# Performance work log

Measured on AMD Instinct MI355X. Metric: run time of the kernel, lower is better.

## Reference

```python
import jax, jax.numpy as jnp
import numpy as np

N_HEAD = 16
D_HEAD = 64
D_MODEL = 1024
LN_EPS = 1e-5


def layer_norm(x, gamma, beta):
    mu = jnp.mean(x, axis=-1, keepdims=True)
    var = jnp.mean((x - mu) ** 2, axis=-1, keepdims=True)
    return (x - mu) * jax.lax.rsqrt(var + LN_EPS) * gamma + beta


def setup_inputs() -> dict:
    key = jax.random.key(0)
    ks = jax.random.split(key, 6)
    B, T = 2, 2048
    inp = jax.random.normal(ks[0], (B, T, D_MODEL), dtype=jnp.float32)
    # qkv_net: Linear(d_model, 3*n_head*d_head)
    W_qkv = jax.random.normal(ks[1], (3 * N_HEAD * D_HEAD, D_MODEL), dtype=jnp.float32) * (D_MODEL ** -0.5)
    b_qkv = jax.random.normal(ks[2], (3 * N_HEAD * D_HEAD,), dtype=jnp.float32) * 0.02
    # o_net: Linear(n_head*d_head, d_model, bias=False)
    W_o = jax.random.normal(ks[3], (D_MODEL, N_HEAD * D_HEAD), dtype=jnp.float32) * ((N_HEAD * D_HEAD) ** -0.5)
    gamma = jnp.ones((D_MODEL,), dtype=jnp.float32)
    beta = jnp.zeros((D_MODEL,), dtype=jnp.float32)
    return {"inp": inp, "W_qkv": W_qkv, "b_qkv": b_qkv, "W_o": W_o, "gamma": gamma, "beta": beta}


def reference(inp, W_qkv, b_qkv, W_o, gamma, beta):
    B, T, D = inp.shape
    H, dh = N_HEAD, D_HEAD
    scale = 1.0 / (dh ** 0.5)

    qkv = inp @ W_qkv.T + b_qkv                      # (B, T, 3*H*dh)
    head_q, head_k, head_v = jnp.split(qkv, 3, axis=2)
    # (B, T, H, dh) -> (B, H, T, dh)
    q = head_q.reshape(B, T, H, dh).transpose(0, 2, 1, 3)
    k = head_k.reshape(B, T, H, dh).transpose(0, 2, 1, 3)
    v = head_v.reshape(B, T, H, dh).transpose(0, 2, 1, 3)

    attn_score = jnp.einsum('bhqd,bhkd->bhqk', q, k) * scale  # (B, H, T, T)
    attn_prob = jax.nn.softmax(attn_score, axis=-1)           # dropatt is identity in eval
    attn_vec = jnp.einsum('bhqk,bhkd->bhqd', attn_prob, v)    # (B, H, T, dh)

    # Faithful to original: (B*H, T, dh) batch-major buffer is VIEWED as (H, B, T, dh)
    attn_vec = attn_vec.reshape(H, B, T, dh)
    attn_vec = attn_vec.transpose(1, 2, 0, 3).reshape(B, T, H * dh)

    attn_out = attn_vec @ W_o.T                                # dropout identity in eval
    return layer_norm(inp + attn_out, gamma, beta)
```

## Files before the change

### kernel.cpp

```cpp
#include <hip/hip_runtime.h>
#include <hip/hip_bf16.h>
#include <stdint.h>

typedef __bf16 bf16_t;
typedef __bf16 bf16x8 __attribute__((ext_vector_type(8)));
typedef __bf16 bf16x4 __attribute__((ext_vector_type(4)));
typedef float floatx4 __attribute__((ext_vector_type(4)));

#define QSCALE 0.180336879f

__device__ static inline void gll16(const void* g, void* l) {
    __builtin_amdgcn_global_load_lds((const __attribute__((address_space(1))) void*)g,
                                     (__attribute__((address_space(3))) void*)l, 16, 0, 0);
}

__global__ __launch_bounds__(256) void cvt_all(const float* __restrict__ inp,
                                               const float* __restrict__ wqkv,
                                               const float* __restrict__ wo,
                                               bf16_t* __restrict__ o_inp,
                                               bf16_t* __restrict__ o_wqkv,
                                               bf16_t* __restrict__ o_wo) {
    int blk = blockIdx.x;
    const float* src;
    bf16_t* dst;
    if (blk < 4096)      { src = inp;  dst = o_inp; }
    else if (blk < 7168) { src = wqkv; dst = o_wqkv; blk -= 4096; }
    else                 { src = wo;   dst = o_wo;   blk -= 7168; }
    int i = blk * 256 + threadIdx.x;
    float4 v = ((const float4*)src)[i];
    bf16x4 o;
    o[0] = (bf16_t)v.x; o[1] = (bf16_t)v.y; o[2] = (bf16_t)v.z; o[3] = (bf16_t)v.w;
    ((bf16x4*)dst)[i] = o;
}

__global__ __launch_bounds__(256, 3)
void gemm_qkv(const bf16_t* __restrict__ A, const bf16_t* __restrict__ Bw,
              const float* __restrict__ bias,
              bf16_t* __restrict__ qk, bf16_t* __restrict__ vT) {
    constexpr int K = 1024;
    __shared__ bf16_t lA[128 * 32];
    __shared__ bf16_t lB[128 * 32];
    const int tid  = threadIdx.x;
    const int lane = tid & 63, wave = tid >> 6;
    const int quad = lane >> 4, l16 = lane & 15;
    const int wy = wave >> 1, wx = wave & 1;
    const int bm = blockIdx.y * 128, bn = blockIdx.x * 128;

    const int c0 = tid, c1 = tid + 256;
    const bf16_t* Ap0 = A + (size_t)(bm + (c0 >> 2)) * K + (c0 & 3) * 8;
    const bf16_t* Ap1 = A + (size_t)(bm + (c1 >> 2)) * K + (c1 & 3) * 8;
    const bf16_t* Bp0 = Bw + (size_t)(bn + (c0 >> 2)) * K + (c0 & 3) * 8;
    const bf16_t* Bp1 = Bw + (size_t)(bn + (c1 >> 2)) * K + (c1 & 3) * 8;
    bf16_t* dA0 = &lA[(wave * 64) * 8];
    bf16_t* dA1 = &lA[(256 + wave * 64) * 8];
    bf16_t* dB0 = &lB[(wave * 64) * 8];
    bf16_t* dB1 = &lB[(256 + wave * 64) * 8];

    floatx4 acc[4][4] = {};

    for (int kt = 0; kt < K; kt += 32) {
        __syncthreads();
        gll16(Ap0 + kt, dA0);
        gll16(Ap1 + kt, dA1);
        gll16(Bp0 + kt, dB0);
        gll16(Bp1 + kt, dB1);
        __syncthreads();
        bf16x8 af[4], bfr[4];
#pragma unroll
        for (int i = 0; i < 4; i++) {
            af[i]  = *(const bf16x8*)(lA + (wy * 64 + i * 16 + l16) * 32 + quad * 8);
            bfr[i] = *(const bf16x8*)(lB + (wx * 64 + i * 16 + l16) * 32 + quad * 8);
        }
#pragma unroll
        for (int i = 0; i < 4; i++)
#pragma unroll
            for (int j = 0; j < 4; j++)
                acc[i][j] = __builtin_amdgcn_mfma_f32_16x16x32_bf16(af[i], bfr[j], acc[i][j], 0, 0, 0);
    }

    const bool is_v = (bn >= 2048);
#pragma unroll
    for (int j = 0; j < 4; j++) {
        const int n = bn + wx * 64 + j * 16 + l16;
        const float bv = bias[n];
        const bool isq = (n < 1024);
#pragma unroll
        for (int i = 0; i < 4; i++) {
            const int mbase = bm + wy * 64 + i * 16 + quad * 4;
            if (!is_v) {
#pragma unroll
                for (int r = 0; r < 4; r++) {
                    float c = acc[i][j][r] + bv;
                    if (isq) c *= QSCALE;
                    qk[(size_t)(mbase + r) * 2048 + n] = (bf16_t)c;
                }
            } else {
                const int nn = n - 2048;
                const int b  = mbase >> 11;
                const int t  = mbase & 2047;
                const int vrow = b * 1024 + nn;
                const int pcol = (t & ~31) | (((t >> 2) & 3) << 3) | (((t >> 4) & 1) << 2);
                bf16x4 pack;
#pragma unroll
                for (int r = 0; r < 4; r++) pack[r] = (bf16_t)(acc[i][j][r] + bv);
                *(bf16x4*)(vT + (size_t)vrow * 2048 + pcol) = pack;
            }
        }
    }
}

__global__ __launch_bounds__(256, 4)
void attn_kernel(const bf16_t* __restrict__ qk, const bf16_t* __restrict__ vT,
                 bf16_t* __restrict__ Opart, float* __restrict__ lpart) {
    __shared__ bf16_t Kbuf[2][64 * 64];
    __shared__ bf16_t Vbuf[2][64 * 64];
    const int tid  = threadIdx.x;
    const int lane = tid & 63, wave = tid >> 6;
    const int quad = lane >> 4, l16 = lane & 15;
    const int bid = blockIdx.x;
    const int s    = bid & 63;
    const int hl   = ((s & 7) << 2) | ((s >> 3) & 3);
    const int half = (s >> 5) & 1;
    const int qt   = bid >> 6;
    const int b = hl >> 4, h = hl & 15;
    const int kt0 = half * 1024;

    const bf16_t* Qbase = qk + (size_t)(b * 2048 + qt * 128 + wave * 32) * 2048 + h * 64;
    const bf16_t* Kbase = qk + (size_t)(b * 2048) * 2048 + 1024 + h * 64;
    const bf16_t* Vbase = vT + (size_t)(hl * 64) * 2048;

    const int srow = tid >> 2, sc8 = (tid & 3) * 8;
    const bf16_t* KgA = Kbase + (size_t)(kt0 + srow) * 2048 + sc8;
    const bf16_t* KgB = KgA + 32;
    const bf16_t* VgA = Vbase + (size_t)srow * 2048 + kt0 + sc8;
    const bf16_t* VgB = VgA + 32;
    const int wbase = wave * 512;

    bf16x8 qf[2][2];
#pragma unroll
    for (int rt = 0; rt < 2; rt++)
#pragma unroll
        for (int kc = 0; kc < 2; kc++)
            qf[rt][kc] = *(const bf16x8*)(Qbase + (size_t)(rt * 16 + l16) * 2048 + kc * 32 + quad * 8);

    floatx4 accO[2][4] = {};
    float lacc[2] = {0.f, 0.f};

    gll16(KgA, &Kbuf[0][wbase]);
    gll16(KgB, &Kbuf[0][2048 + wbase]);
    gll16(VgA, &Vbuf[0][wbase]);
    gll16(VgB, &Vbuf[0][2048 + wbase]);

    for (int it = 0; it < 16; ++it) {
        const int cur = it & 1, nxt = cur ^ 1;
        __syncthreads();
        if (it < 15) {
            const size_t ko = (size_t)(it + 1) * 64 * 2048;
            const int    vo = (it + 1) * 64;
            gll16(KgA + ko, &Kbuf[nxt][wbase]);
            gll16(KgB + ko, &Kbuf[nxt][2048 + wbase]);
            gll16(VgA + vo, &Vbuf[nxt][wbase]);
            gll16(VgB + vo, &Vbuf[nxt][2048 + wbase]);
        }
        floatx4 st[2][4] = {};
#pragma unroll
        for (int nt = 0; nt < 4; nt++) {
            bf16x8 k0 = *(const bf16x8*)&Kbuf[cur][(nt * 16 + l16) * 32 + quad * 8];
            bf16x8 k1 = *(const bf16x8*)&Kbuf[cur][2048 + (nt * 16 + l16) * 32 + quad * 8];
            st[0][nt] = __builtin_amdgcn_mfma_f32_16x16x32_bf16(k0, qf[0][0], st[0][nt], 0, 0, 0);
            st[0][nt] = __builtin_amdgcn_mfma_f32_16x16x32_bf16(k1, qf[0][1], st[0][nt], 0, 0, 0);
            st[1][nt] = __builtin_amdgcn_mfma_f32_16x16x32_bf16(k0, qf[1][0], st[1][nt], 0, 0, 0);
            st[1][nt] = __builtin_amdgcn_mfma_f32_16x16x32_bf16(k1, qf[1][1], st[1][nt], 0, 0, 0);
        }
#pragma unroll
        for (int kc2 = 0; kc2 < 2; kc2++) {
            bf16x8 vf[4];
#pragma unroll
            for (int ct = 0; ct < 4; ct++)
                vf[ct] = *(const bf16x8*)&Vbuf[cur][kc2 * 2048 + (ct * 16 + l16) * 32 + quad * 8];
#pragma unroll
            for (int rt = 0; rt < 2; rt++) {
                bf16x8 pf;
                float ls = 0.f;
#pragma unroll
                for (int j = 0; j < 8; j++) {
                    float p = __builtin_amdgcn_exp2f(st[rt][kc2 * 2 + (j >> 2)][j & 3]);
                    ls += p;
                    pf[j] = (bf16_t)p;
                }
                lacc[rt] += ls;
#pragma unroll
                for (int ct = 0; ct < 4; ct++)
                    accO[rt][ct] = __builtin_amdgcn_mfma_f32_16x16x32_bf16(pf, vf[ct], accO[rt][ct], 0, 0, 0);
            }
        }
    }

    float lsum[2];
#pragma unroll
    for (int rt = 0; rt < 2; rt++) {
        float l = lacc[rt];
        l += __shfl_xor(l, 16);
        l += __shfl_xor(l, 32);
        lsum[rt] = l;
    }
    const int b2 = hl & 1;
    const int colb = hl >> 1;
    const int rowb = b2 * 2048 + qt * 128 + wave * 32;
    bf16_t* outb = Opart + (size_t)half * (4096 * 1024) + (size_t)rowb * 1024 + colb * 64;
#pragma unroll
    for (int rt = 0; rt < 2; rt++)
#pragma unroll
        for (int ct = 0; ct < 4; ct++)
#pragma unroll
            for (int r = 0; r < 4; r++)
                outb[(size_t)(rt * 16 + quad * 4 + r) * 1024 + ct * 16 + l16] = (bf16_t)(accO[rt][ct][r]);
    if (quad == 0) {
#pragma unroll
        for (int rt = 0; rt < 2; rt++)
            lpart[half * 65536 + (rowb + rt * 16 + l16) * 16 + colb] = lsum[rt];
    }
}

__global__ __launch_bounds__(256, 4)
void gemm_o(const bf16_t* __restrict__ Op, const float* __restrict__ lp,
            const bf16_t* __restrict__ Bw, float* __restrict__ out) {
    constexpr int K = 1024;
    __shared__ bf16_t lA[64 * 32];
    __shared__ bf16_t lB[128 * 32];
    const int tid  = threadIdx.x;
    const int lane = tid & 63, wave = tid >> 6;
    const int quad = lane >> 4, l16 = lane & 15;
    const int wy = wave >> 1, wx = wave & 1;
    const int bm = blockIdx.y * 64, bn = blockIdx.x * 128;

    const int ca = tid;
    const int arow = bm + (ca >> 2);
    const int ak   = (ca & 3) * 8;
    const bf16_t* Ap0 = Op + (size_t)arow * 1024 + ak;
    const bf16_t* Ap1 = Ap0 + (size_t)4096 * 1024;
    const float*  lrow = lp + arow * 16;
    const int cb0 = tid, cb1 = tid + 256;
    const bf16_t* Bp0 = Bw + (size_t)(bn + (cb0 >> 2)) * K + (cb0 & 3) * 8;
    const bf16_t* Bp1 = Bw + (size_t)(bn + (cb1 >> 2)) * K + (cb1 & 3) * 8;
    bf16_t* dB0 = &lB[(wave * 64) * 8];
    bf16_t* dB1 = &lB[(256 + wave * 64) * 8];

    floatx4 acc[2][4] = {};
    for (int kt = 0; kt < K; kt += 32) {
        bf16x8 a0 = *(const bf16x8*)(Ap0 + kt);
        bf16x8 a1 = *(const bf16x8*)(Ap1 + kt);
        const int cb = (kt + ak) >> 6;
        const float inv = 1.0f / (lrow[cb] + lrow[65536 + cb]);
        bf16x8 av;
#pragma unroll
        for (int j = 0; j < 8; j++)
            av[j] = (bf16_t)(((float)a0[j] + (float)a1[j]) * inv);
        __syncthreads();
        gll16(Bp0 + kt, dB0);
        gll16(Bp1 + kt, dB1);
        *(bf16x8*)&lA[ca * 8] = av;
        __syncthreads();
        bf16x8 af[2], bfr[4];
#pragma unroll
        for (int i = 0; i < 2; i++)
            af[i] = *(const bf16x8*)(lA + (wy * 32 + i * 16 + l16) * 32 + quad * 8);
#pragma unroll
        for (int j = 0; j < 4; j++)
            bfr[j] = *(const bf16x8*)(lB + (wx * 64 + j * 16 + l16) * 32 + quad * 8);
#pragma unroll
        for (int i = 0; i < 2; i++)
#pragma unroll
            for (int j = 0; j < 4; j++)
                acc[i][j] = __builtin_amdgcn_mfma_f32_16x16x32_bf16(af[i], bfr[j], acc[i][j], 0, 0, 0);
    }
#pragma unroll
    for (int j = 0; j < 4; j++) {
        const int n = bn + wx * 64 + j * 16 + l16;
#pragma unroll
        for (int i = 0; i < 2; i++) {
            const int mbase = bm + wy * 32 + i * 16 + quad * 4;
#pragma unroll
            for (int r = 0; r < 4; r++)
                out[(size_t)(mbase + r) * 1024 + n] = acc[i][j][r];
        }
    }
}

__global__ __launch_bounds__(256)
void ln_kernel(const float* __restrict__ inp, const float* __restrict__ ao,
               const float* __restrict__ gamma, const float* __restrict__ beta,
               float* __restrict__ out) {
    const int row = blockIdx.x, tid = threadIdx.x;
    const int wave = tid >> 6, lane = tid & 63;
    float4 a = ((const float4*)(inp + (size_t)row * 1024))[tid];
    float4 c = ((const float4*)(ao + (size_t)row * 1024))[tid];
    float x0 = a.x + c.x, x1 = a.y + c.y, x2 = a.z + c.z, x3 = a.w + c.w;
    float s = x0 + x1 + x2 + x3;
    float sq = x0 * x0 + x1 * x1 + x2 * x2 + x3 * x3;
#pragma unroll
    for (int mm = 32; mm >= 1; mm >>= 1) {
        s += __shfl_xor(s, mm);
        sq += __shfl_xor(sq, mm);
    }
    __shared__ float rs[4], rq[4];
    if (lane == 0) { rs[wave] = s; rq[wave] = sq; }
    __syncthreads();
    s = rs[0] + rs[1] + rs[2] + rs[3];
    sq = rq[0] + rq[1] + rq[2] + rq[3];
    const float mu = s * (1.0f / 1024.0f);
    const float var = sq * (1.0f / 1024.0f) - mu * mu;
    const float rstd = rsqrtf(var + 1e-5f);
    float4 g = ((const float4*)gamma)[tid], bt = ((const float4*)beta)[tid];
    float4 o;
    o.x = (x0 - mu) * rstd * g.x + bt.x;
    o.y = (x1 - mu) * rstd * g.y + bt.y;
    o.z = (x2 - mu) * rstd * g.z + bt.z;
    o.w = (x3 - mu) * rstd * g.w + bt.w;
    ((float4*)(out + (size_t)row * 1024))[tid] = o;
}

extern "C" void kernel_launch(void* const* d_in, const int* in_sizes, int n_in,
                              void* d_out, int out_size, void* d_ws, size_t ws_size,
                              hipStream_t stream) {
    const float* inp   = (const float*)d_in[0];
    const float* Wqkv  = (const float*)d_in[1];
    const float* bqkv  = (const float*)d_in[2];
    const float* Wo    = (const float*)d_in[3];
    const float* gamma = (const float*)d_in[4];
    const float* beta  = (const float*)d_in[5];
    float* out = (float*)d_out;

    char* ws = (char*)d_ws;
    bf16_t* inp_bf  = (bf16_t*)(ws);
    bf16_t* wqkv_bf = (bf16_t*)(ws + (8u << 20));
    bf16_t* wo_bf   = (bf16_t*)(ws + (14u << 20));
    bf16_t* qk_buf  = (bf16_t*)(ws + (16u << 20));
    bf16_t* vT_buf  = (bf16_t*)(ws + (32u << 20));
    float*  ao_buf  = (float*)(ws + (32u << 20));
    bf16_t* opart   = (bf16_t*)(ws + (48u << 20));
    float*  lpart   = (float*)(ws);

    cvt_all<<<8192, 256, 0, stream>>>(inp, Wqkv, Wo, inp_bf, wqkv_bf, wo_bf);
    gemm_qkv<<<dim3(24, 32), 256, 0, stream>>>(inp_bf, wqkv_bf, bqkv, qk_buf, vT_buf);
    attn_kernel<<<1024, 256, 0, stream>>>(qk_buf, vT_buf, opart, lpart);
    gemm_o<<<dim3(8, 64), 256, 0, stream>>>(opart, lpart, wo_bf, ao_buf);
    ln_kernel<<<4096, 256, 0, stream>>>(inp, ao_buf, gamma, beta, out);
}
```

Baseline: 204.2 us.

## Use packed bf16 conversion, prefetch gemm_o A tiles, store attention output in bf16

Adds a pack8 helper that uses the packed f32-to-bf16 convert builtin when it is available, and applies it in cvt_all, in the attention softmax-to-MFMA path and in gemm_o. gemm_o now loads the next A-operand chunk from global memory after the barrier, so the load overlaps the MFMA work. The o-projection result is also written as bf16 instead of fp32, which halves that intermediate's write and the layer-norm read of it. The bf16 intermediate loses precision before the residual add and layer norm.

```diff
diff --git a/kernel.cpp b/kernel.cpp
--- a/kernel.cpp
+++ b/kernel.cpp
@@ -5,13 +5,33 @@
 typedef __bf16 bf16_t;
 typedef __bf16 bf16x8 __attribute__((ext_vector_type(8)));
 typedef __bf16 bf16x4 __attribute__((ext_vector_type(4)));
+typedef __bf16 bf16x2 __attribute__((ext_vector_type(2)));
 typedef float floatx4 __attribute__((ext_vector_type(4)));
 
 #define QSCALE 0.180336879f
+
+#if __has_builtin(__builtin_amdgcn_cvt_pk_bf16_f32)
+#define HAS_PK_BF16 1
+#endif
 
 __device__ static inline void gll16(const void* g, void* l) {
     __builtin_amdgcn_global_load_lds((const __attribute__((address_space(1))) void*)g,
                                      (__attribute__((address_space(3))) void*)l, 16, 0, 0);
+}
+
+__device__ static inline bf16x8 pack8(const float* p) {
+    bf16x8 o;
+#ifdef HAS_PK_BF16
+#pragma unroll
+    for (int j = 0; j < 4; j++) {
+        bf16x2 t2 = __builtin_amdgcn_cvt_pk_bf16_f32(p[2 * j], p[2 * j + 1]);
+        o[2 * j] = t2[0]; o[2 * j + 1] = t2[1];
+    }
+#else
+#pragma unroll
+    for (int j = 0; j < 8; j++) o[j] = (bf16_t)p[j];
+#endif
+    return o;
 }
 
 __global__ __launch_bounds__(256) void cvt_all(const float* __restrict__ inp,
@@ -28,8 +48,15 @@
     else                 { src = wo;   dst = o_wo;   blk -= 7168; }
     int i = blk * 256 + threadIdx.x;
     float4 v = ((const float4*)src)[i];
+    float p[4] = {v.x, v.y, v.z, v.w};
     bf16x4 o;
-    o[0] = (bf16_t)v.x; o[1] = (bf16_t)v.y; o[2] = (bf16_t)v.z; o[3] = (bf16_t)v.w;
+#ifdef HAS_PK_BF16
+    bf16x2 t0 = __builtin_amdgcn_cvt_pk_bf16_f32(p[0], p[1]);
+    bf16x2 t1 = __builtin_amdgcn_cvt_pk_bf16_f32(p[2], p[3]);
+    o[0] = t0[0]; o[1] = t0[1]; o[2] = t1[0]; o[3] = t1[1];
+#else
+    o[0] = (bf16_t)p[0]; o[1] = (bf16_t)p[1]; o[2] = (bf16_t)p[2]; o[3] = (bf16_t)p[3];
+#endif
     ((bf16x4*)dst)[i] = o;
 }
 
@@ -180,15 +207,15 @@
                 vf[ct] = *(const bf16x8*)&Vbuf[cur][kc2 * 2048 + (ct * 16 + l16) * 32 + quad * 8];
 #pragma unroll
             for (int rt = 0; rt < 2; rt++) {
-                bf16x8 pf;
+                float p[8];
                 float ls = 0.f;
 #pragma unroll
                 for (int j = 0; j < 8; j++) {
-                    float p = __builtin_amdgcn_exp2f(st[rt][kc2 * 2 + (j >> 2)][j & 3]);
-                    ls += p;
-                    pf[j] = (bf16_t)p;
+                    p[j] = __builtin_amdgcn_exp2f(st[rt][kc2 * 2 + (j >> 2)][j & 3]);
+                    ls += p[j];
                 }
                 lacc[rt] += ls;
+                bf16x8 pf = pack8(p);
 #pragma unroll
                 for (int ct = 0; ct < 4; ct++)
                     accO[rt][ct] = __builtin_amdgcn_mfma_f32_16x16x32_bf16(pf, vf[ct], accO[rt][ct], 0, 0, 0);
@@ -224,7 +251,7 @@
 
 __global__ __launch_bounds__(256, 4)
 void gemm_o(const bf16_t* __restrict__ Op, const float* __restrict__ lp,
-            const bf16_t* __restrict__ Bw, float* __restrict__ out) {
+            const bf16_t* __restrict__ Bw, bf16_t* __restrict__ out) {
     constexpr int K = 1024;
     __shared__ bf16_t lA[64 * 32];
     __shared__ bf16_t lB[128 * 32];
@@ -246,21 +273,26 @@
     bf16_t* dB0 = &lB[(wave * 64) * 8];
     bf16_t* dB1 = &lB[(256 + wave * 64) * 8];
 
+    bf16x8 a0 = *(const bf16x8*)(Ap0);
+    bf16x8 a1 = *(const bf16x8*)(Ap1);
+
     floatx4 acc[2][4] = {};
     for (int kt = 0; kt < K; kt += 32) {
-        bf16x8 a0 = *(const bf16x8*)(Ap0 + kt);
-        bf16x8 a1 = *(const bf16x8*)(Ap1 + kt);
         const int cb = (kt + ak) >> 6;
         const float inv = 1.0f / (lrow[cb] + lrow[65536 + cb]);
-        bf16x8 av;
-#pragma unroll
-        for (int j = 0; j < 8; j++)
-            av[j] = (bf16_t)(((float)a0[j] + (float)a1[j]) * inv);
+        float p[8];
+#pragma unroll
+        for (int j = 0; j < 8; j++) p[j] = ((float)a0[j] + (float)a1[j]) * inv;
+        bf16x8 av = pack8(p);
         __syncthreads();
         gll16(Bp0 + kt, dB0);
         gll16(Bp1 + kt, dB1);
         *(bf16x8*)&lA[ca * 8] = av;
         __syncthreads();
+        if (kt + 32 < K) {
+            a0 = *(const bf16x8*)(Ap0 + kt + 32);
+            a1 = *(const bf16x8*)(Ap1 + kt + 32);
+        }
         bf16x8 af[2], bfr[4];
 #pragma unroll
         for (int i = 0; i < 2; i++)
@@ -282,20 +314,21 @@
             const int mbase = bm + wy * 32 + i * 16 + quad * 4;
 #pragma unroll
             for (int r = 0; r < 4; r++)
-                out[(size_t)(mbase + r) * 1024 + n] = acc[i][j][r];
+                out[(size_t)(mbase + r) * 1024 + n] = (bf16_t)acc[i][j][r];
         }
     }
 }
 
 __global__ __launch_bounds__(256)
-void ln_kernel(const float* __restrict__ inp, const float* __restrict__ ao,
+void ln_kernel(const float* __restrict__ inp, const bf16_t* __restrict__ ao,
                const float* __restrict__ gamma, const float* __restrict__ beta,
                float* __restrict__ out) {
     const int row = blockIdx.x, tid = threadIdx.x;
     const int wave = tid >> 6, lane = tid & 63;
     float4 a = ((const float4*)(inp + (size_t)row * 1024))[tid];
-    float4 c = ((const float4*)(ao + (size_t)row * 1024))[tid];
-    float x0 = a.x + c.x, x1 = a.y + c.y, x2 = a.z + c.z, x3 = a.w + c.w;
+    bf16x4 c4 = ((const bf16x4*)(ao + (size_t)row * 1024))[tid];
+    float x0 = a.x + (float)c4[0], x1 = a.y + (float)c4[1];
+    float x2 = a.z + (float)c4[2], x3 = a.w + (float)c4[3];
     float s = x0 + x1 + x2 + x3;
     float sq = x0 * x0 + x1 * x1 + x2 * x2 + x3 * x3;
 #pragma unroll
@@ -337,13 +370,13 @@
     bf16_t* wo_bf   = (bf16_t*)(ws + (14u << 20));
     bf16_t* qk_buf  = (bf16_t*)(ws + (16u << 20));
     bf16_t* vT_buf  = (bf16_t*)(ws + (32u << 20));
-    float*  ao_buf  = (float*)(ws + (32u << 20));
+    bf16_t* ao_bf   = (bf16_t*)(ws + (32u << 20));
     bf16_t* opart   = (bf16_t*)(ws + (48u << 20));
     float*  lpart   = (float*)(ws);
 
     cvt_all<<<8192, 256, 0, stream>>>(inp, Wqkv, Wo, inp_bf, wqkv_bf, wo_bf);
     gemm_qkv<<<dim3(24, 32), 256, 0, stream>>>(inp_bf, wqkv_bf, bqkv, qk_buf, vT_buf);
     attn_kernel<<<1024, 256, 0, stream>>>(qk_buf, vT_buf, opart, lpart);
-    gemm_o<<<dim3(8, 64), 256, 0, stream>>>(opart, lpart, wo_bf, ao_buf);
-    ln_kernel<<<4096, 256, 0, stream>>>(inp, ao_buf, gamma, beta, out);
-}
+    gemm_o<<<dim3(8, 64), 256, 0, stream>>>(opart, lpart, wo_bf, ao_bf);
+    ln_kernel<<<4096, 256, 0, stream>>>(inp, ao_bf, gamma, beta, out);
+}
```

Result: no change. 205.3 us (+0.5%).
